# Optimization experiments

Measured on AMD Instinct MI355X. Metric: run time of the kernel, lower is better.

Reference implementation:

```python
import jax, jax.numpy as jnp
import numpy as np

N = 100_000      # nodes
E = 3_200_000    # edges (avg degree 32)
F_IN = 172       # raw node features
HID = 32         # hid_channels
ENC = 8          # encoding_dim
H, C = 2, 16     # heads, per-head channels (TransformerConv 32 -> 2x16)
OUT = 2          # classes
INV_SQRT_C = 1.0 / np.sqrt(C).astype(np.float32)


def setup_inputs() -> dict:
    key = jax.random.key(0)
    ks = jax.random.split(key, 40)
    p = lambda k, shape: (jax.random.normal(k, shape, dtype=jnp.float32) * 0.05)
    return {
        # data tensors
        "x": jax.random.normal(ks[0], (N, F_IN), dtype=jnp.float32),
        "edge_index": jax.random.randint(ks[1], (2, E), 0, N),
        "node_time": jax.random.uniform(ks[2], (N,), dtype=jnp.float32),
        "edge_time": jax.random.uniform(ks[3], (E, 1), dtype=jnp.float32),
        "node_interval": jax.random.uniform(ks[4], (N, 1), dtype=jnp.float32),
        "node_degree": jax.random.uniform(ks[5], (N, 1), dtype=jnp.float32),
        # TimeEncode(32): cos(Linear(1, 32))
        "Wt": p(ks[6], (1, HID)), "bt": p(ks[7], (HID,)),
        # DegreeEncoder / TemporalFrequencyEncoder: Linear(1, 8)
        "Wd": p(ks[8], (1, ENC)), "bd": p(ks[9], (ENC,)),
        "Wtf": p(ks[10], (1, ENC)), "btf": p(ks[11], (ENC,)),
        # w_enc: Linear(8, 8); w_x: Linear(32, 8)
        "Wenc": p(ks[12], (ENC, ENC)), "benc": p(ks[13], (ENC,)),
        "Wx": p(ks[14], (HID, ENC)), "bx": p(ks[15], (ENC,)),
        # lin: Linear(in_channels, 32)
        "Wlin": p(ks[16], (F_IN, HID)), "blin": p(ks[17], (HID,)),
        # lin_combine: Linear(40, 32)
        "Wcomb": p(ks[18], (HID + ENC, HID)), "bcomb": p(ks[19], (HID,)),
        # TransformerConv projections (32 -> heads*16 = 32)
        "Wq": p(ks[20], (HID, H * C)), "bq": p(ks[21], (H * C,)),
        "Wk": p(ks[22], (HID, H * C)), "bk": p(ks[23], (H * C,)),
        "Wv": p(ks[24], (HID, H * C)), "bv": p(ks[25], (H * C,)),
        "We": p(ks[26], (HID, H * C)), "be": p(ks[27], (H * C,)),
        "Wskip": p(ks[28], (HID, H * C)), "bskip": p(ks[29], (H * C,)),
        # out: Linear(32, out_channels)
        "Wout": p(ks[30], (HID, OUT)), "bout": p(ks[31], (OUT,)),
    }


def _segment_softmax(alpha, seg, num_segments):
    # alpha: [E, H], seg: [E] destination indices
    m = jax.ops.segment_max(alpha, seg, num_segments=num_segments)
    a = jnp.exp(alpha - m[seg])
    s = jax.ops.segment_sum(a, seg, num_segments=num_segments)
    return a / (s[seg] + 1e-16)


def reference(x, edge_index, node_time, edge_time, node_interval, node_degree,
              Wt, bt, Wd, bd, Wtf, btf, Wenc, benc, Wx, bx, Wlin, blin,
              Wcomb, bcomb, Wq, bq, Wk, bk, Wv, bv, We, be, Wskip, bskip,
              Wout, bout):
    src, dst = edge_index[0], edge_index[1]
    n = x.shape[0]

    # ---- time encoding of relative edge time: cos(Linear(rel_t)) ----
    rel_t = node_time[src][:, None] - edge_time               # [E, 1]
    rel_t_enc = jnp.cos(rel_t @ Wt + bt)                      # [E, 32]

    # ---- node encoders + attention-gated combine ----
    h1 = x @ Wlin + blin                                      # [N, 32]
    tf_enc = node_interval @ Wtf + btf                        # [N, 8]
    deg_enc = node_degree @ Wd + bd                           # [N, 8]
    encodings = jnp.stack((tf_enc, deg_enc), axis=1)          # [N, 2, 8]
    enc_proj = jnp.tanh(encodings @ Wenc + benc)              # [N, 2, 8]
    x_proj = jnp.tanh(h1 @ Wx + bx)                           # [N, 8]
    score = jnp.einsum('nke,ne->nk', enc_proj, x_proj)        # [N, 2]
    score = jax.nn.softmax(score, axis=1)
    context = jnp.einsum('nke,nk->ne', encodings, score)      # [N, 8]
    h1 = jnp.concatenate((h1, context), axis=1) @ Wcomb + bcomb  # [N, 32]

    # ---- TransformerConv (heads=2, out=16, concat) with edge features ----
    q = (h1 @ Wq + bq).reshape(n, H, C)
    k = (h1 @ Wk + bk).reshape(n, H, C)
    v = (h1 @ Wv + bv).reshape(n, H, C)
    e = (rel_t_enc @ We + be).reshape(-1, H, C)               # [E, H, C]

    k_e = k[src] + e                                          # [E, H, C]
    alpha = jnp.einsum('ehc,ehc->eh', q[dst], k_e) * INV_SQRT_C
    alpha = _segment_softmax(alpha, dst, n)                   # [E, H]
    msg = (v[src] + e) * alpha[..., None]                     # [E, H, C]
    agg = jax.ops.segment_sum(msg, dst, num_segments=n)       # [N, H, C]
    h2 = agg.reshape(n, H * C) + (h1 @ Wskip + bskip)         # root_weight skip

    out = h2 @ Wout + bout                                    # [N, 2]
    return jax.nn.log_softmax(out, axis=1)
```

## Files before the change

### kernel.cpp

```cpp
#include <hip/hip_runtime.h>
#include <hip/hip_bf16.h>
#include <cstdint>


#define FIN 172
#define INV_SQRT_C 0.25f

typedef _Float16 f16x8 __attribute__((ext_vector_type(8)));
typedef float f32x4 __attribute__((ext_vector_type(4)));

__device__ __forceinline__ uint32_t cvt_pk_bf16(float lo, float hi) {
    uint32_t r;
    asm("v_cvt_pk_bf16_f32 %0, %1, %2" : "=v"(r) : "v"(lo), "v"(hi));
    return r;
}

__device__ __forceinline__ void pk_atomic_add_bf16(void* addr, uint32_t data) {
    asm volatile("global_atomic_pk_add_bf16 %0, %1, off"
                 :: "v"((uint64_t)(uintptr_t)addr), "v"(data) : "memory");
}

__global__ __launch_bounds__(256) void k1_lin(
    const float* __restrict__ x, const float* __restrict__ Wlin,
    const float* __restrict__ blin, float* __restrict__ h1pre, int n)
{
    __shared__ __align__(16) float WlT[32][174];
    __shared__ __align__(16) float xs[8][FIN];
    const int t = threadIdx.x;

    for (int i = t; i < FIN * 32; i += 256) {
        int kk = i >> 5, o = i & 31;
        WlT[o][kk] = Wlin[i];
    }
    const int row0 = blockIdx.x * 8;
    for (int i = t; i < 8 * FIN; i += 256) {
        int rr = i / FIN, kk = i - rr * FIN;
        int gr = row0 + rr;
        xs[rr][kk] = (gr < n) ? x[(size_t)gr * FIN + kk] : 0.f;
    }
    __syncthreads();

    const int o = t & 31, r = t >> 5;
    float acc = blin[o];
    const float2* wp = reinterpret_cast<const float2*>(&WlT[o][0]);
    const float2* xp = reinterpret_cast<const float2*>(&xs[r][0]);
    #pragma unroll 4
    for (int kk = 0; kk < FIN / 2; ++kk) {
        float2 wv = wp[kk], xv = xp[kk];
        acc = fmaf(xv.x, wv.x, acc);
        acc = fmaf(xv.y, wv.y, acc);
    }
    const int gr = row0 + r;
    if (gr < n) h1pre[(size_t)gr * 32 + o] = acc;
}

template <int K, int O>
__device__ __forceinline__ void matvecKO(const float* __restrict__ v,
                                         const float* __restrict__ W,
                                         const float* __restrict__ B,
                                         float* __restrict__ out)
{
    #pragma unroll
    for (int o4 = 0; o4 < O / 4; ++o4) {
        float a0 = B[o4 * 4 + 0], a1 = B[o4 * 4 + 1];
        float a2 = B[o4 * 4 + 2], a3 = B[o4 * 4 + 3];
        #pragma unroll
        for (int k = 0; k < K; ++k) {
            float4 wv = *reinterpret_cast<const float4*>(&W[k * O + o4 * 4]);
            float hv = v[k];
            a0 = fmaf(hv, wv.x, a0);
            a1 = fmaf(hv, wv.y, a1);
            a2 = fmaf(hv, wv.z, a2);
            a3 = fmaf(hv, wv.w, a3);
        }
        out[o4 * 4 + 0] = a0; out[o4 * 4 + 1] = a1;
        out[o4 * 4 + 2] = a2; out[o4 * 4 + 3] = a3;
    }
}

__device__ __forceinline__ void store32(float* __restrict__ dst,
                                        const float* __restrict__ v)
{
    float4* d4 = reinterpret_cast<float4*>(dst);
    #pragma unroll
    for (int i = 0; i < 8; ++i)
        d4[i] = make_float4(v[4 * i], v[4 * i + 1], v[4 * i + 2], v[4 * i + 3]);
}

__global__ __launch_bounds__(256) void k2_enc(
    const float* __restrict__ h1pre,
    const float* __restrict__ node_interval, const float* __restrict__ node_degree,
    const float* __restrict__ Wtf, const float* __restrict__ btf,
    const float* __restrict__ Wd,  const float* __restrict__ bd,
    const float* __restrict__ Wenc, const float* __restrict__ benc,
    const float* __restrict__ Wx,  const float* __restrict__ bx,
    const float* __restrict__ Wcomb, const float* __restrict__ bcomb,
    const float* __restrict__ Wq,  const float* __restrict__ bq,
    const float* __restrict__ Wk,  const float* __restrict__ bk,
    const float* __restrict__ Wv,  const float* __restrict__ bv,
    const float* __restrict__ Wskip, const float* __restrict__ bskip,
    float* __restrict__ qb, float* __restrict__ kb, float* __restrict__ vb,
    float* __restrict__ skipb, int n)
{
    __shared__ __align__(16) float sWenc[64], sWx[256], sWcomb[1280];
    __shared__ __align__(16) float sWq[1024], sWk[1024], sWv[1024], sWs[1024];
    __shared__ float sWtf[8], sbtf[8], sWd[8], sbd[8], sbenc[8], sbx[8];
    __shared__ float sbcomb[32], sbq[32], sbk[32], sbv[32], sbs[32];

    const int t = threadIdx.x;
    if (t < 8) {
        sWtf[t] = Wtf[t]; sbtf[t] = btf[t];
        sWd[t]  = Wd[t];  sbd[t]  = bd[t];
        sbenc[t] = benc[t]; sbx[t] = bx[t];
    }
    if (t < 32) {
        sbcomb[t] = bcomb[t]; sbq[t] = bq[t]; sbk[t] = bk[t];
        sbv[t] = bv[t]; sbs[t] = bskip[t];
    }
    if (t < 64) sWenc[t] = Wenc[t];
    if (t < 256) sWx[t] = Wx[t];
    for (int i = t; i < 1280; i += 256) sWcomb[i] = Wcomb[i];
    for (int i = t; i < 1024; i += 256) {
        sWq[i] = Wq[i]; sWk[i] = Wk[i]; sWv[i] = Wv[i]; sWs[i] = Wskip[i];
    }
    __syncthreads();

    const int nid = blockIdx.x * 256 + t;
    if (nid >= n) return;

    float h1p[32];
    {
        const float2* hp = reinterpret_cast<const float2*>(h1pre + (size_t)nid * 32);
        #pragma unroll
        for (int i = 0; i < 16; ++i) {
            float2 v2 = hp[i];
            h1p[2 * i] = v2.x; h1p[2 * i + 1] = v2.y;
        }
    }
    const float ti = node_interval[nid], dg = node_degree[nid];
    float tf[8], de[8];
    #pragma unroll
    for (int j = 0; j < 8; ++j) {
        tf[j] = fmaf(ti, sWtf[j], sbtf[j]);
        de[j] = fmaf(dg, sWd[j], sbd[j]);
    }
    float xp[8];
    matvecKO<32, 8>(h1p, sWx, sbx, xp);
    #pragma unroll
    for (int o = 0; o < 8; ++o) xp[o] = tanhf(xp[o]);

    float ep0[8], ep1[8];
    matvecKO<8, 8>(tf, sWenc, sbenc, ep0);
    matvecKO<8, 8>(de, sWenc, sbenc, ep1);
    float sc0 = 0.f, sc1 = 0.f;
    #pragma unroll
    for (int o = 0; o < 8; ++o) {
        sc0 = fmaf(tanhf(ep0[o]), xp[o], sc0);
        sc1 = fmaf(tanhf(ep1[o]), xp[o], sc1);
    }
    const float mm = fmaxf(sc0, sc1);
    const float e0 = __expf(sc0 - mm), e1 = __expf(sc1 - mm);
    const float inv = 1.f / (e0 + e1);
    const float s0 = e0 * inv, s1 = e1 * inv;

    float v40[40];
    #pragma unroll
    for (int i = 0; i < 32; ++i) v40[i] = h1p[i];
    #pragma unroll
    for (int j = 0; j < 8; ++j) v40[32 + j] = fmaf(s0, tf[j], s1 * de[j]);
    float h1[32];
    matvecKO<40, 32>(v40, sWcomb, sbcomb, h1);

    float tmp[32];
    matvecKO<32, 32>(h1, sWq, sbq, tmp); store32(qb   + (size_t)nid * 32, tmp);
    matvecKO<32, 32>(h1, sWk, sbk, tmp); store32(kb   + (size_t)nid * 32, tmp);
    matvecKO<32, 32>(h1, sWv, sbv, tmp); store32(vb   + (size_t)nid * 32, tmp);
    matvecKO<32, 32>(h1, sWs, sbs, tmp); store32(skipb + (size_t)nid * 32, tmp);
}

__global__ __launch_bounds__(256) void k3_edge(
    const int* __restrict__ ei, const float* __restrict__ node_time,
    const float* __restrict__ edge_time,
    const float* __restrict__ qb, const float* __restrict__ kb,
    const float* __restrict__ vb,
    const float* __restrict__ Wt, const float* __restrict__ bt,
    const float* __restrict__ We, const float* __restrict__ be,
    unsigned short* __restrict__ agg, float* __restrict__ den,
    int numE, int nTiles)
{
    const int lane = threadIdx.x & 63;
    const int g = lane >> 4;
    const int m = lane & 15;

    float wtr[8], btr[8];
    f16x8 B0, B1;
    #pragma unroll
    for (int i = 0; i < 8; ++i) {
        const int k = g * 8 + i;
        wtr[i] = Wt[k];
        btr[i] = bt[k];
        B0[i] = (_Float16)We[k * 32 + m];
        B1[i] = (_Float16)We[k * 32 + 16 + m];
    }
    const float be0 = be[m], be1 = be[16 + m];

    const int wid    = blockIdx.x * (blockDim.x >> 6) + (threadIdx.x >> 6);
    const int nWaves = gridDim.x * (blockDim.x >> 6);

    for (int tile = wid; tile < nTiles; tile += nWaves) {
        const int e0 = tile * 16;
        const int eA = e0 + m;
        int srcm = 0, dstm = 0;
        float rel = 0.f;
        if (eA < numE) {
            srcm = ei[eA];
            dstm = ei[numE + eA];
            rel  = node_time[srcm] - edge_time[eA];
        }

        f16x8 A;
        #pragma unroll
        for (int i = 0; i < 8; ++i)
            A[i] = (_Float16)__cosf(fmaf(rel, wtr[i], btr[i]));

        f32x4 acc0 = {0.f, 0.f, 0.f, 0.f};
        f32x4 acc1 = {0.f, 0.f, 0.f, 0.f};
        acc0 = __builtin_amdgcn_mfma_f32_16x16x32_f16(A, B0, acc0, 0, 0, 0);
        acc1 = __builtin_amdgcn_mfma_f32_16x16x32_f16(A, B1, acc1, 0, 0, 0);

        #pragma unroll
        for (int r = 0; r < 4; ++r) {
            const int j = g * 4 + r;
            const int e = e0 + j;
            if (e < numE) {
                const int srcr = __shfl(srcm, j);
                const int dstr = __shfl(dstm, j);

                const float ef0 = acc0[r] + be0;
                const float ef1 = acc1[r] + be1;

                const size_t sb = (size_t)srcr * 32;
                const size_t db = (size_t)dstr * 32;
                const float q0 = qb[db + m],      q1 = qb[db + 16 + m];
                const float k0 = kb[sb + m],      k1 = kb[sb + 16 + m];
                const float v0 = vb[sb + m],      v1 = vb[sb + 16 + m];

                float p0 = q0 * (k0 + ef0);
                float p1 = q1 * (k1 + ef1);
                #pragma unroll
                for (int s = 1; s < 16; s <<= 1) {
                    p0 += __shfl_xor(p0, s);
                    p1 += __shfl_xor(p1, s);
                }
                const float w0 = __expf(p0 * INV_SQRT_C);
                const float w1 = __expf(p1 * INV_SQRT_C);

                const float t0 = w0 * (v0 + ef0);
                const float t1 = w1 * (v1 + ef1);
                const float x0 = __shfl_xor(t0, 1);
                const float x1 = __shfl_xor(t1, 1);
                const uint32_t dE = cvt_pk_bf16(t0, x0);
                const uint32_t dO = cvt_pk_bf16(x1, t1);
                const uint32_t data = (m & 1) ? dO : dE;
                const int choff = (m & 1) ? (15 + m) : m;
                pk_atomic_add_bf16(agg + db + choff, data);

                if (m < 2) atomicAdd(&den[(size_t)dstr * 2 + m], m ? w1 : w0);
            }
        }
    }
}

__global__ __launch_bounds__(256) void k4_out(
    const unsigned short* __restrict__ agg, const float* __restrict__ den,
    const float* __restrict__ skipb,
    const float* __restrict__ Wout, const float* __restrict__ bout,
    float* __restrict__ out, int n)
{
    __shared__ float sW[64];
    __shared__ float sb[2];
    const int t = threadIdx.x;
    if (t < 64) sW[t] = Wout[t];
    if (t < 2) sb[t] = bout[t];
    __syncthreads();

    const int nid = blockIdx.x * 256 + t;
    if (nid >= n) return;

    const float inv0 = 1.f / (den[(size_t)nid * 2 + 0] + 1e-16f);
    const float inv1 = 1.f / (den[(size_t)nid * 2 + 1] + 1e-16f);
    const uint32_t* ag = reinterpret_cast<const uint32_t*>(agg) + (size_t)nid * 16;
    const float4*  sk4 = reinterpret_cast<const float4*>(skipb + (size_t)nid * 32);

    float o0 = sb[0], o1 = sb[1];
    #pragma unroll
    for (int p = 0; p < 16; ++p) {
        const uint32_t u = ag[p];
        const float aLo = __uint_as_float(u << 16);
        const float aHi = __uint_as_float(u & 0xFFFF0000u);
        const float iv = (p < 8) ? inv0 : inv1;
        const float s0 = reinterpret_cast<const float*>(sk4)[2 * p];
        const float s1 = reinterpret_cast<const float*>(sk4)[2 * p + 1];
        const float hLo = fmaf(aLo, iv, s0);
        const float hHi = fmaf(aHi, iv, s1);
        o0 = fmaf(hLo, sW[(2 * p) * 2],     o0);
        o1 = fmaf(hLo, sW[(2 * p) * 2 + 1], o1);
        o0 = fmaf(hHi, sW[(2 * p + 1) * 2],     o0);
        o1 = fmaf(hHi, sW[(2 * p + 1) * 2 + 1], o1);
    }
    const float mm = fmaxf(o0, o1);
    const float lse = mm + __logf(__expf(o0 - mm) + __expf(o1 - mm));
    out[(size_t)nid * 2 + 0] = o0 - lse;
    out[(size_t)nid * 2 + 1] = o1 - lse;
}

extern "C" void kernel_launch(void* const* d_in, const int* in_sizes, int n_in,
                              void* d_out, int out_size, void* d_ws, size_t ws_size,
                              hipStream_t stream)
{
    const float* x             = (const float*)d_in[0];
    const int*   ei            = (const int*)  d_in[1];
    const float* node_time     = (const float*)d_in[2];
    const float* edge_time     = (const float*)d_in[3];
    const float* node_interval = (const float*)d_in[4];
    const float* node_degree   = (const float*)d_in[5];
    const float* Wt    = (const float*)d_in[6];  const float* bt    = (const float*)d_in[7];
    const float* Wd    = (const float*)d_in[8];  const float* bd    = (const float*)d_in[9];
    const float* Wtf   = (const float*)d_in[10]; const float* btf   = (const float*)d_in[11];
    const float* Wenc  = (const float*)d_in[12]; const float* benc  = (const float*)d_in[13];
    const float* Wx    = (const float*)d_in[14]; const float* bx    = (const float*)d_in[15];
    const float* Wlin  = (const float*)d_in[16]; const float* blin  = (const float*)d_in[17];
    const float* Wcomb = (const float*)d_in[18]; const float* bcomb = (const float*)d_in[19];
    const float* Wq    = (const float*)d_in[20]; const float* bq    = (const float*)d_in[21];
    const float* Wk    = (const float*)d_in[22]; const float* bk    = (const float*)d_in[23];
    const float* Wv    = (const float*)d_in[24]; const float* bv    = (const float*)d_in[25];
    const float* We    = (const float*)d_in[26]; const float* be    = (const float*)d_in[27];
    const float* Wskip = (const float*)d_in[28]; const float* bskip = (const float*)d_in[29];
    const float* Wout  = (const float*)d_in[30]; const float* bout  = (const float*)d_in[31];

    const int n    = in_sizes[2];
    const int numE = in_sizes[3];

    char* base = (char*)d_ws;
    float* qb    = (float*)base; base += (size_t)n * 32 * 4;
    float* kb    = (float*)base; base += (size_t)n * 32 * 4;
    float* vb    = (float*)base; base += (size_t)n * 32 * 4;
    float* skipb = (float*)base; base += (size_t)n * 32 * 4;
    float* h1pre = (float*)base; base += (size_t)n * 32 * 4;
    unsigned short* agg = (unsigned short*)base; base += (size_t)n * 32 * 2;
    float* den   = (float*)base; base += (size_t)n * 2 * 4;

    hipMemsetAsync(agg, 0, (size_t)n * (32 * 2 + 2 * 4), stream);

    k1_lin<<<(n + 7) / 8, 256, 0, stream>>>(x, Wlin, blin, h1pre, n);

    k2_enc<<<(n + 255) / 256, 256, 0, stream>>>(
        h1pre, node_interval, node_degree,
        Wtf, btf, Wd, bd, Wenc, benc, Wx, bx, Wcomb, bcomb,
        Wq, bq, Wk, bk, Wv, bv, Wskip, bskip,
        qb, kb, vb, skipb, n);

    const int nTiles = (numE + 15) / 16;
    k3_edge<<<2048, 256, 0, stream>>>(
        ei, node_time, edge_time, qb, kb, vb,
        Wt, bt, We, be, agg, den, numE, nTiles);

    k4_out<<<(n + 255) / 256, 256, 0, stream>>>(
        agg, den, skipb, Wout, bout, (float*)d_out, n);
}
```

Measured before the change: 508.8 us.

## Store q/k/v in bf16 with interleaved k|v rows and double k1 rows per block

Node-level q, k and v projections are now written as packed bf16, with k and v interleaved into one 64-element row per source node, instead of three separate fp32 buffers. The edge kernel gathers these halved-size rows, which cuts random-gather bandwidth and puts k and v for a source node in the same cache lines. The linear kernel also handles 16 rows per block with two accumulators, so each shared-memory weight load is reused twice. The cost is bf16 rounding of q/k/v, which adds error to the attention logits.

```diff
diff --git a/kernel.cpp b/kernel.cpp
--- a/kernel.cpp
+++ b/kernel.cpp
@@ -15,6 +15,12 @@
     return r;
 }
 
+__device__ __forceinline__ float bf2f(unsigned short u) {
+    union { uint32_t i; float f; } x;
+    x.i = ((uint32_t)u) << 16;
+    return x.f;
+}
+
 __device__ __forceinline__ void pk_atomic_add_bf16(void* addr, uint32_t data) {
     asm volatile("global_atomic_pk_add_bf16 %0, %1, off"
                  :: "v"((uint64_t)(uintptr_t)addr), "v"(data) : "memory");
@@ -25,15 +31,15 @@
     const float* __restrict__ blin, float* __restrict__ h1pre, int n)
 {
     __shared__ __align__(16) float WlT[32][174];
-    __shared__ __align__(16) float xs[8][FIN];
+    __shared__ __align__(16) float xs[16][FIN];
     const int t = threadIdx.x;
 
     for (int i = t; i < FIN * 32; i += 256) {
         int kk = i >> 5, o = i & 31;
         WlT[o][kk] = Wlin[i];
     }
-    const int row0 = blockIdx.x * 8;
-    for (int i = t; i < 8 * FIN; i += 256) {
+    const int row0 = blockIdx.x * 16;
+    for (int i = t; i < 16 * FIN; i += 256) {
         int rr = i / FIN, kk = i - rr * FIN;
         int gr = row0 + rr;
         xs[rr][kk] = (gr < n) ? x[(size_t)gr * FIN + kk] : 0.f;
@@ -41,17 +47,21 @@
     __syncthreads();
 
     const int o = t & 31, r = t >> 5;
-    float acc = blin[o];
-    const float2* wp = reinterpret_cast<const float2*>(&WlT[o][0]);
-    const float2* xp = reinterpret_cast<const float2*>(&xs[r][0]);
+    float acc0 = blin[o], acc1 = acc0;
+    const float2* wp  = reinterpret_cast<const float2*>(&WlT[o][0]);
+    const float2* xp0 = reinterpret_cast<const float2*>(&xs[r][0]);
+    const float2* xp1 = reinterpret_cast<const float2*>(&xs[r + 8][0]);
     #pragma unroll 4
     for (int kk = 0; kk < FIN / 2; ++kk) {
-        float2 wv = wp[kk], xv = xp[kk];
-        acc = fmaf(xv.x, wv.x, acc);
-        acc = fmaf(xv.y, wv.y, acc);
-    }
-    const int gr = row0 + r;
-    if (gr < n) h1pre[(size_t)gr * 32 + o] = acc;
+        float2 wv = wp[kk], xa = xp0[kk], xb = xp1[kk];
+        acc0 = fmaf(xa.x, wv.x, acc0);
+        acc0 = fmaf(xa.y, wv.y, acc0);
+        acc1 = fmaf(xb.x, wv.x, acc1);
+        acc1 = fmaf(xb.y, wv.y, acc1);
+    }
+    const int g0 = row0 + r, g1 = row0 + r + 8;
+    if (g0 < n) h1pre[(size_t)g0 * 32 + o] = acc0;
+    if (g1 < n) h1pre[(size_t)g1 * 32 + o] = acc1;
 }
 
 template <int K, int O>
@@ -99,7 +109,7 @@
     const float* __restrict__ Wk,  const float* __restrict__ bk,
     const float* __restrict__ Wv,  const float* __restrict__ bv,
     const float* __restrict__ Wskip, const float* __restrict__ bskip,
-    float* __restrict__ qb, float* __restrict__ kb, float* __restrict__ vb,
+    uint32_t* __restrict__ q32, uint32_t* __restrict__ kv32,
     float* __restrict__ skipb, int n)
 {
     __shared__ __align__(16) float sWenc[64], sWx[256], sWcomb[1280];
@@ -171,18 +181,27 @@
     float h1[32];
     matvecKO<40, 32>(v40, sWcomb, sbcomb, h1);
 
-    float tmp[32];
-    matvecKO<32, 32>(h1, sWq, sbq, tmp); store32(qb   + (size_t)nid * 32, tmp);
-    matvecKO<32, 32>(h1, sWk, sbk, tmp); store32(kb   + (size_t)nid * 32, tmp);
-    matvecKO<32, 32>(h1, sWv, sbv, tmp); store32(vb   + (size_t)nid * 32, tmp);
-    matvecKO<32, 32>(h1, sWs, sbs, tmp); store32(skipb + (size_t)nid * 32, tmp);
+    float tq[32], tk[32], tv[32], ts[32];
+    matvecKO<32, 32>(h1, sWq, sbq, tq);
+    matvecKO<32, 32>(h1, sWk, sbk, tk);
+    matvecKO<32, 32>(h1, sWv, sbv, tv);
+    matvecKO<32, 32>(h1, sWs, sbs, ts);
+
+    uint32_t* qw  = q32  + (size_t)nid * 16;
+    uint32_t* kvw = kv32 + (size_t)nid * 32;
+    #pragma unroll
+    for (int p = 0; p < 16; ++p) {
+        qw[p]       = cvt_pk_bf16(tq[2 * p], tq[2 * p + 1]);
+        kvw[p]      = cvt_pk_bf16(tk[2 * p], tk[2 * p + 1]);
+        kvw[16 + p] = cvt_pk_bf16(tv[2 * p], tv[2 * p + 1]);
+    }
+    store32(skipb + (size_t)nid * 32, ts);
 }
 
 __global__ __launch_bounds__(256) void k3_edge(
     const int* __restrict__ ei, const float* __restrict__ node_time,
     const float* __restrict__ edge_time,
-    const float* __restrict__ qb, const float* __restrict__ kb,
-    const float* __restrict__ vb,
+    const unsigned short* __restrict__ qbh, const unsigned short* __restrict__ kvb,
     const float* __restrict__ Wt, const float* __restrict__ bt,
     const float* __restrict__ We, const float* __restrict__ be,
     unsigned short* __restrict__ agg, float* __restrict__ den,
@@ -239,11 +258,11 @@
                 const float ef0 = acc0[r] + be0;
                 const float ef1 = acc1[r] + be1;
 
-                const size_t sb = (size_t)srcr * 32;
-                const size_t db = (size_t)dstr * 32;
-                const float q0 = qb[db + m],      q1 = qb[db + 16 + m];
-                const float k0 = kb[sb + m],      k1 = kb[sb + 16 + m];
-                const float v0 = vb[sb + m],      v1 = vb[sb + 16 + m];
+                const unsigned short* qs  = qbh + (size_t)dstr * 32;
+                const unsigned short* kvs = kvb + (size_t)srcr * 64;
+                const float q0 = bf2f(qs[m]),       q1 = bf2f(qs[16 + m]);
+                const float k0 = bf2f(kvs[m]),      k1 = bf2f(kvs[16 + m]);
+                const float v0 = bf2f(kvs[32 + m]), v1 = bf2f(kvs[48 + m]);
 
                 float p0 = q0 * (k0 + ef0);
                 float p1 = q1 * (k1 + ef1);
@@ -263,6 +282,7 @@
                 const uint32_t dO = cvt_pk_bf16(x1, t1);
                 const uint32_t data = (m & 1) ? dO : dE;
                 const int choff = (m & 1) ? (15 + m) : m;
+                const size_t db = (size_t)dstr * 32;
                 pk_atomic_add_bf16(agg + db + choff, data);
 
                 if (m < 2) atomicAdd(&den[(size_t)dstr * 2 + m], m ? w1 : w0);
@@ -290,7 +310,7 @@
     const float inv0 = 1.f / (den[(size_t)nid * 2 + 0] + 1e-16f);
     const float inv1 = 1.f / (den[(size_t)nid * 2 + 1] + 1e-16f);
     const uint32_t* ag = reinterpret_cast<const uint32_t*>(agg) + (size_t)nid * 16;
-    const float4*  sk4 = reinterpret_cast<const float4*>(skipb + (size_t)nid * 32);
+    const float*    sk = skipb + (size_t)nid * 32;
 
     float o0 = sb[0], o1 = sb[1];
     #pragma unroll
@@ -299,10 +319,8 @@
         const float aLo = __uint_as_float(u << 16);
         const float aHi = __uint_as_float(u & 0xFFFF0000u);
         const float iv = (p < 8) ? inv0 : inv1;
-        const float s0 = reinterpret_cast<const float*>(sk4)[2 * p];
-        const float s1 = reinterpret_cast<const float*>(sk4)[2 * p + 1];
-        const float hLo = fmaf(aLo, iv, s0);
-        const float hHi = fmaf(aHi, iv, s1);
+        const float hLo = fmaf(aLo, iv, sk[2 * p]);
+        const float hHi = fmaf(aHi, iv, sk[2 * p + 1]);
         o0 = fmaf(hLo, sW[(2 * p) * 2],     o0);
         o1 = fmaf(hLo, sW[(2 * p) * 2 + 1], o1);
         o0 = fmaf(hHi, sW[(2 * p + 1) * 2],     o0);
@@ -342,9 +360,8 @@
     const int numE = in_sizes[3];
 
     char* base = (char*)d_ws;
-    float* qb    = (float*)base; base += (size_t)n * 32 * 4;
-    float* kb    = (float*)base; base += (size_t)n * 32 * 4;
-    float* vb    = (float*)base; base += (size_t)n * 32 * 4;
+    unsigned short* qbh = (unsigned short*)base; base += (size_t)n * 32 * 2;
+    unsigned short* kvb = (unsigned short*)base; base += (size_t)n * 64 * 2;
     float* skipb = (float*)base; base += (size_t)n * 32 * 4;
     float* h1pre = (float*)base; base += (size_t)n * 32 * 4;
     unsigned short* agg = (unsigned short*)base; base += (size_t)n * 32 * 2;
@@ -352,17 +369,17 @@
 
     hipMemsetAsync(agg, 0, (size_t)n * (32 * 2 + 2 * 4), stream);
 
-    k1_lin<<<(n + 7) / 8, 256, 0, stream>>>(x, Wlin, blin, h1pre, n);
+    k1_lin<<<(n + 15) / 16, 256, 0, stream>>>(x, Wlin, blin, h1pre, n);
 
     k2_enc<<<(n + 255) / 256, 256, 0, stream>>>(
         h1pre, node_interval, node_degree,
         Wtf, btf, Wd, bd, Wenc, benc, Wx, bx, Wcomb, bcomb,
         Wq, bq, Wk, bk, Wv, bv, Wskip, bskip,
-        qb, kb, vb, skipb, n);
+        (uint32_t*)qbh, (uint32_t*)kvb, skipb, n);
 
     const int nTiles = (numE + 15) / 16;
     k3_edge<<<2048, 256, 0, stream>>>(
-        ei, node_time, edge_time, qb, kb, vb,
+        ei, node_time, edge_time, qbh, kvb,
         Wt, bt, We, be, agg, den, numE, nTiles);
 
     k4_out<<<(n + 255) / 256, 256, 0, stream>>>(
```

Result: no change. 515.7 us (+1.4%).
